# Performance work log

Hardware: AMD Instinct MI355X
Metric: run time of the kernel (lower is better)

The kernel has to match this reference:

```python
import jax, jax.numpy as jnp
import numpy as np

NEG_INF = -1000000.0
G = 8            # window size (hardcoded: assert 8*8 == N)
DIM = 28         # hardcoded channel dim
NH = 4           # num_heads
HD = DIM // NH   # head dim = 7
PDIM = (DIM // 4) // 4  # DynamicPosBias pos_dim = (28//4)//4 = 1


def layernorm(x, g, b, eps=1e-5):
    m = jnp.mean(x, axis=-1, keepdims=True)
    v = jnp.mean((x - m) ** 2, axis=-1, keepdims=True)
    return (x - m) * jax.lax.rsqrt(v + eps) * g + b


def setup_inputs() -> dict:
    key = jax.random.key(0)
    ks = jax.random.split(key, 16)
    s = 0.05
    inp = {
        "x": jax.random.normal(ks[0], (8, 250, 250, DIM), jnp.float32),
        "qkv_w": jax.random.normal(ks[1], (3 * DIM, DIM), jnp.float32) * s,
        "qkv_b": jnp.zeros((3 * DIM,), jnp.float32),
        "proj_w": jax.random.normal(ks[2], (DIM, DIM), jnp.float32) * s,
        "proj_b": jnp.zeros((DIM,), jnp.float32),
        "pos_proj_w": jax.random.normal(ks[3], (PDIM, 2), jnp.float32) * s,
        "pos_proj_b": jnp.zeros((PDIM,), jnp.float32),
        "ln1_g": jnp.ones((PDIM,), jnp.float32),
        "ln1_b": jnp.zeros((PDIM,), jnp.float32),
        "fc1_w": jax.random.normal(ks[4], (PDIM, PDIM), jnp.float32) * s,
        "fc1_b": jnp.zeros((PDIM,), jnp.float32),
        "ln2_g": jnp.ones((PDIM,), jnp.float32),
        "ln2_b": jnp.zeros((PDIM,), jnp.float32),
        "fc2_w": jax.random.normal(ks[5], (PDIM, PDIM), jnp.float32) * s,
        "fc2_b": jnp.zeros((PDIM,), jnp.float32),
        "ln3_g": jnp.ones((PDIM,), jnp.float32),
        "ln3_b": jnp.zeros((PDIM,), jnp.float32),
        "fc3_w": jax.random.normal(ks[6], (NH, PDIM), jnp.float32) * s,
        "fc3_b": jnp.zeros((NH,), jnp.float32),
    }
    return inp


def _rel_pos_index():
    # static relative position index table, (G*G, G*G) int32 in [0, (2G-1)^2)
    coords = np.stack(np.meshgrid(np.arange(G), np.arange(G), indexing="ij"))  # (2,G,G)
    cf = coords.reshape(2, -1)                                                  # (2,GG)
    rel = cf[:, :, None] - cf[:, None, :]                                       # (2,GG,GG)
    rel = rel.transpose(1, 2, 0)
    rel[:, :, 0] += G - 1
    rel[:, :, 1] += G - 1
    rel[:, :, 0] *= 2 * G - 1
    return jnp.asarray(rel.sum(-1), jnp.int32)


def _biases():
    # (2G-1)^2 candidate relative offsets, float (225, 2)
    ph = np.arange(1 - G, G)
    b = np.stack(np.meshgrid(ph, ph, indexing="ij")).reshape(2, -1).T
    return jnp.asarray(b, jnp.float32)


def reference(x, qkv_w, qkv_b, proj_w, proj_b,
              pos_proj_w, pos_proj_b,
              ln1_g, ln1_b, fc1_w, fc1_b,
              ln2_g, ln2_b, fc2_w, fc2_b,
              ln3_g, ln3_b, fc3_w, fc3_b):
    B, H, W, C = x.shape
    pad_b = (-H) % G
    pad_r = (-W) % G
    x = jnp.pad(x, ((0, 0), (0, pad_b), (0, pad_r), (0, 0)))
    Hd, Wd = H + pad_b, W + pad_r
    nH, nW = Hd // G, Wd // G
    nP = nH * nW
    GG = G * G

    # window partition -> (B*nP, GG, C)
    xw = x.reshape(B, nH, G, nW, G, C).transpose(0, 1, 3, 2, 4, 5).reshape(B * nP, GG, C)

    # padding mask over keys, per window: (nP, 1, GG) additive
    m2d = jnp.zeros((Hd, Wd), jnp.float32)
    if pad_b > 0:
        m2d = m2d.at[-pad_b:, :].set(-1.0)
    if pad_r > 0:
        m2d = m2d.at[:, -pad_r:].set(-1.0)
    mw = m2d.reshape(nH, G, nW, G).transpose(0, 2, 1, 3).reshape(nP, GG)
    attn_mask = jnp.where(mw[:, None, :] < 0, NEG_INF, 0.0)  # (nP,1,GG)

    # qkv projection
    qkv = xw @ qkv_w.T + qkv_b                    # (B_, GG, 3C)
    qkv = qkv.reshape(B * nP, GG, 3, NH, HD).transpose(2, 0, 3, 1, 4)
    q, k, v = qkv[0], qkv[1], qkv[2]              # (B_, NH, GG, HD)
    scale = HD ** (-0.5)
    attn = jnp.einsum("bhnd,bhmd->bhnm", q * scale, k)  # (B_, NH, GG, GG)

    # dynamic relative position bias: tiny MLP over (2G-1)^2 offsets
    t = _biases() @ pos_proj_w.T + pos_proj_b                      # (225, PDIM)
    t = layernorm(t, ln1_g, ln1_b)
    t = jax.nn.relu(t) @ fc1_w.T + fc1_b
    t = layernorm(t, ln2_g, ln2_b)
    t = jax.nn.relu(t) @ fc2_w.T + fc2_b
    t = layernorm(t, ln3_g, ln3_b)
    pos = jax.nn.relu(t) @ fc3_w.T + fc3_b                         # (225, NH)
    rpb = pos[_rel_pos_index()]                                    # (GG, GG, NH)
    rpb = rpb.transpose(2, 0, 1)                                   # (NH, GG, GG)
    attn = attn + rpb[None]

    # add padding mask then softmax
    attn = attn.reshape(B, nP, NH, GG, GG) + attn_mask[None, :, None, :, :]
    attn = jax.nn.softmax(attn.reshape(B * nP, NH, GG, GG), axis=-1)

    out = jnp.einsum("bhnm,bhmd->bnhd", attn, v).reshape(B * nP, GG, C)
    out = out @ proj_w.T + proj_b

    # un-window, crop padding, flatten spatial
    out = out.reshape(B, nH, nW, G, G, C).transpose(0, 1, 3, 2, 4, 5).reshape(B, Hd, Wd, C)
    out = out[:, :H, :W, :].reshape(B, H * W, C)
    return out
```

## Files before the change

### kernel.cpp

```cpp
#include <hip/hip_runtime.h>

#define HW 250

typedef float    f32x16 __attribute__((ext_vector_type(16)));
typedef _Float16 f16x8  __attribute__((ext_vector_type(8)));
typedef unsigned u32x4  __attribute__((ext_vector_type(4)));

__device__ inline unsigned pkrtz(float a, float b) {
    return __builtin_bit_cast(unsigned, __builtin_amdgcn_cvt_pkrtz(a, b));
}
__device__ inline f16x8 as_f16x8(u32x4 v) { return __builtin_bit_cast(f16x8, v); }

#define OFF_X   0
#define OFF_WA  2560
#define OFF_PW  7680
#define OFF_VT  8960


__global__ __launch_bounds__(256, 7)
void win_attn(const float* __restrict__ x,
              const float* __restrict__ qkv_w,
              const float* __restrict__ qkv_b,
              const float* __restrict__ proj_w,
              const float* __restrict__ proj_b,
              float* __restrict__ out)
{
    __shared__ __align__(16) short s_pool[11008];
    __shared__ __align__(16) float s_pb[28];
    short* const s_x16  = s_pool + OFF_X;
    short* const s_wa   = s_pool + OFF_WA;
    short* const s_pw16 = s_pool + OFF_PW;
    short* const s_vt   = s_pool + OFF_VT;
    short* const s_o16  = s_pool + OFF_X;
    float* const s_of   = (float*)(s_pool + OFF_WA);

    const int t    = threadIdx.x;
    const int lane = t & 63;
    const int w    = t >> 6;
    const int s_   = lane >> 5;
    const int col  = lane & 31;
    const int blk = blockIdx.x;
    const int b   = blk >> 10;
    const int p   = blk & 1023;
    const int r0  = (p >> 5) << 3;
    const int c0  = (p & 31) << 3;

    f32x16 Z;
    #pragma unroll
    for (int r = 0; r < 16; ++r) Z[r] = 0.f;

    {
        const int co = t >> 3, g = t & 7;
        uint2 h; h.x = 0u; h.y = 0u;
        if (g < 7) {
            if (co < 28) {
                const float4 v = *(const float4*)&proj_w[co * 28 + g * 4];
                h.x = pkrtz(v.x, v.y); h.y = pkrtz(v.z, v.w);
            }
            *(uint2*)&s_pw16[co * 40 + g * 4] = h;
        } else {
            *(uint2*)&s_pw16[co * 40 + 28] = h;
        }
    }
    if (t < 28) s_pb[t] = proj_b[t];

    #pragma unroll
    for (int it = 0; it < 2; ++it) {
        const int i = t + it * 256;
        const int n = i >> 3, g = i & 7;
        if (g < 7) {
            const int r = r0 + (n >> 3), c = c0 + (n & 7);
            float4 v = make_float4(0.f, 0.f, 0.f, 0.f);
            if (r < HW && c < HW)
                v = *(const float4*)&x[((b * HW + r) * HW + c) * 28 + g * 4];
            uint2 h; h.x = pkrtz(v.x, v.y); h.y = pkrtz(v.z, v.w);
            *(uint2*)&s_x16[n * 40 + g * 4] = h;
        } else {
            uint2 h; h.x = 0x00003C00u; h.y = 0u;
            *(uint2*)&s_x16[n * 40 + 28] = h;
        }
    }

    {
        const int rowid = t >> 1, half = t & 1;
        const int slab = rowid >> 5, a = rowid & 31;
        const float SC = 0.5452538663326288f;
        int src = -1; float sc = 1.f;
        if      (a < 4)             { src = slab * 7 + a;            sc = SC; }
        else if (a < 8)             { src = 56 + slab * 7 + (a - 4); }
        else if (a < 11)            { src = slab * 7 + (a - 4);      sc = SC; }
        else if (a >= 12 && a < 15) { src = 56 + slab * 7 + (a - 8); }
        else if (a >= 16 && a < 20) { src = 28 + slab * 7 + (a - 16); }
        else if (a >= 24 && a < 27) { src = 28 + slab * 7 + (a - 20); }
        u32x4 o0 = {0u,0u,0u,0u}, o1 = {0u,0u,0u,0u};
        if (src >= 0) {
            const float* wr = &qkv_w[src * 28];
            if (half == 0) {
                const float4 A = *(const float4*)&wr[0],  B = *(const float4*)&wr[4];
                const float4 C = *(const float4*)&wr[8],  D = *(const float4*)&wr[12];
                o0.x = pkrtz(A.x*sc, A.y*sc); o0.y = pkrtz(A.z*sc, A.w*sc);
                o0.z = pkrtz(B.x*sc, B.y*sc); o0.w = pkrtz(B.z*sc, B.w*sc);
                o1.x = pkrtz(C.x*sc, C.y*sc); o1.y = pkrtz(C.z*sc, C.w*sc);
                o1.z = pkrtz(D.x*sc, D.y*sc); o1.w = pkrtz(D.z*sc, D.w*sc);
            } else {
                const float4 A = *(const float4*)&wr[16], B = *(const float4*)&wr[20];
                const float4 C = *(const float4*)&wr[24];
                const float bias = qkv_b[src];
                o0.x = pkrtz(A.x*sc, A.y*sc); o0.y = pkrtz(A.z*sc, A.w*sc);
                o0.z = pkrtz(B.x*sc, B.y*sc); o0.w = pkrtz(B.z*sc, B.w*sc);
                o1.x = pkrtz(C.x*sc, C.y*sc); o1.y = pkrtz(C.z*sc, C.w*sc);
                o1.z = pkrtz(bias*sc, 0.f);   o1.w = 0u;
            }
        }
        *(u32x4*)&s_wa[rowid * 40 + half * 16 + 0] = o0;
        *(u32x4*)&s_wa[rowid * 40 + half * 16 + 8] = o1;
    }
    __syncthreads();

    u32x4 qf0, qf1, kf0, kf1;
    {
        const f16x8 wfa = *(const f16x8*)&s_wa[(w * 32 + col) * 40 + s_ * 8];
        const f16x8 wfb = *(const f16x8*)&s_wa[(w * 32 + col) * 40 + 16 + s_ * 8];
        #pragma unroll
        for (int tile = 0; tile < 2; ++tile) {
            const int tok = tile * 32 + col;
            const f16x8 xb0 = *(const f16x8*)&s_x16[tok * 40 + s_ * 8];
            const f16x8 xb1 = *(const f16x8*)&s_x16[tok * 40 + 16 + s_ * 8];
            f32x16 C;
            C = __builtin_amdgcn_mfma_f32_32x32x16_f16(wfa, xb0, Z, 0, 0, 0);
            C = __builtin_amdgcn_mfma_f32_32x32x16_f16(wfb, xb1, C, 0, 0, 0);
            u32x4 qf, kf;
            qf.x = s_ ? 0u : pkrtz(C[0],  C[1]);
            qf.y = s_ ? 0u : pkrtz(C[2],  C[3]);
            qf.z = s_ ? 0u : pkrtz(C[4],  C[5]);
            qf.w = s_ ? 0u : pkrtz(C[6],  0.f);
            kf.x = s_ ? 0u : pkrtz(C[8],  C[9]);
            kf.y = s_ ? 0u : pkrtz(C[10], C[11]);
            kf.z = s_ ? 0u : pkrtz(C[12], C[13]);
            kf.w = s_ ? 0u : pkrtz(C[14], 0.f);
            if (s_) {
                const int pos = ((tok >> 4) << 4) + (((tok >> 2) & 1) << 3)
                              + (tok & 3) + (((tok >> 3) & 1) << 2);
                #pragma unroll
                for (int d = 0; d < 8; ++d) {
                    const unsigned hv = (d == 7) ? 0x00003C00u : pkrtz(C[d], 0.f);
                    s_vt[w * 512 + ((d * 64 + pos) ^ (d << 3))] = (short)(hv & 0xffff);
                }
            }
            if (tile == 0) { qf0 = qf; kf0 = kf; } else { qf1 = qf; kf1 = kf; }
        }
    }
    __syncthreads();

    {
        const int vr = min(8, HW - r0), vc = min(8, HW - c0);
        const bool edge = (vr < 8) || (vc < 8);
        const int dd = (col < 8) ? col : 6;
        const f16x8 kfa = as_f16x8(kf0), kfb = as_f16x8(kf1);

        #pragma unroll
        for (int qt = 0; qt < 2; ++qt) {
            const f16x8 qfrag = as_f16x8(qt == 0 ? qf0 : qf1);
            f32x16 a0 = __builtin_amdgcn_mfma_f32_32x32x16_f16(kfa, qfrag, Z, 0, 0, 0);
            f32x16 a1 = __builtin_amdgcn_mfma_f32_32x32x16_f16(kfb, qfrag, Z, 0, 0, 0);
            if (edge) {
                #pragma unroll
                for (int r = 0; r < 16; ++r) {
                    const int kc  = (r & 3) + 4 * s_;
                    const int kr0 = (r >> 2), kr1 = 4 + (r >> 2);
                    a0[r] = (kr0 < vr && kc < vc) ? a0[r] : -1e30f;
                    a1[r] = (kr1 < vr && kc < vc) ? a1[r] : -1e30f;
                }
            }
            #pragma unroll
            for (int r = 0; r < 16; ++r) {
                a0[r] = __builtin_amdgcn_exp2f(a0[r]);
                a1[r] = __builtin_amdgcn_exp2f(a1[r]);
            }

            f32x16 O;
            #pragma unroll
            for (int tt = 0; tt < 4; ++tt) {
                const f16x8 vfrag = *(const f16x8*)&s_vt[w * 512 + ((dd * 64 + tt * 16 + s_ * 8) ^ (dd << 3))];
                const int bb = 8 * (tt & 1);
                float p0,p1,p2,p3,p4,p5,p6,p7;
                if (tt < 2) { p0=a0[bb+0];p1=a0[bb+1];p2=a0[bb+2];p3=a0[bb+3];
                              p4=a0[bb+4];p5=a0[bb+5];p6=a0[bb+6];p7=a0[bb+7]; }
                else        { p0=a1[bb+0];p1=a1[bb+1];p2=a1[bb+2];p3=a1[bb+3];
                              p4=a1[bb+4];p5=a1[bb+5];p6=a1[bb+6];p7=a1[bb+7]; }
                u32x4 pf;
                pf.x = pkrtz(p0, p1); pf.y = pkrtz(p2, p3);
                pf.z = pkrtz(p4, p5); pf.w = pkrtz(p6, p7);
                O = __builtin_amdgcn_mfma_f32_32x32x16_f16(vfrag, as_f16x8(pf),
                                                           (tt == 0) ? Z : O, 0, 0, 0);
            }
            const float os = O[3];
            const float prt = __shfl_xor(os, 32);
            const float sum = s_ ? os : prt;
            const float inv = __builtin_amdgcn_rcpf(sum);
            #pragma unroll
            for (int r = 0; r < 4; ++r) {
                const int d = r + 4 * s_;
                if (d < 7) {
                    const unsigned hv = pkrtz(O[r] * inv, 0.f);
                    s_o16[(32 * qt + col) * 40 + w * 7 + d] = (short)(hv & 0xffff);
                }
            }
        }
    }
    __syncthreads();

    {
        const int tile = w & 1, ch = w >> 1;
        const int tok  = tile * 32 + col;
        const f16x8 ob0 = *(const f16x8*)&s_o16[tok * 40 + 8 * s_];
        const f16x8 ob1 = *(const f16x8*)&s_o16[tok * 40 + 16 + 8 * s_];
        const f16x8 wa0 = *(const f16x8*)&s_pw16[col * 40 + 8 * s_];
        const f16x8 wa1 = *(const f16x8*)&s_pw16[col * 40 + 16 + 8 * s_];
        f32x16 C;
        C = __builtin_amdgcn_mfma_f32_32x32x16_f16(wa0, ob0, Z, 0, 0, 0);
        C = __builtin_amdgcn_mfma_f32_32x32x16_f16(wa1, ob1, C, 0, 0, 0);
        const int wr = tok >> 3, tc = tok & 7;
        #pragma unroll
        for (int j2 = 0; j2 < 2; ++j2) {
            const int j  = 2 * ch + j2;
            const int co = 8 * j + 4 * s_;
            if (co < 28) {
                float4 o;
                o.x = C[4*j+0]; o.y = C[4*j+1]; o.z = C[4*j+2]; o.w = C[4*j+3];
                *(float4*)&s_of[wr * 232 + tc * 28 + co] = o;
            }
        }
    }
    __syncthreads();

    {
        const int l7 = lane / 7;
        #pragma unroll
        for (int i = 0; i < 2; ++i) {
            const int wr = 2 * w + i;
            const int rr = r0 + wr;
            if (lane < 56 && rr < HW) {
                const int tc = l7;
                const int c  = 4 * (lane - 7 * tc);
                if (c0 + tc < HW) {
                    float4 o = *(const float4*)&s_of[wr * 232 + 4 * lane];
                    const float4 bias = *(const float4*)&s_pb[c];
                    o.x += bias.x; o.y += bias.y; o.z += bias.z; o.w += bias.w;
                    *(float4*)&out[((b * HW + rr) * HW + c0 + tc) * 28 + c] = o;
                }
            }
        }
    }
}

extern "C" void kernel_launch(void* const* d_in, const int* in_sizes, int n_in,
                              void* d_out, int out_size, void* d_ws, size_t ws_size,
                              hipStream_t stream) {
    const float* x      = (const float*)d_in[0];
    const float* qkv_w  = (const float*)d_in[1];
    const float* qkv_b  = (const float*)d_in[2];
    const float* proj_w = (const float*)d_in[3];
    const float* proj_b = (const float*)d_in[4];
    float* out = (float*)d_out;

    dim3 grid(8 * 32 * 32);
    dim3 block(256);
    hipLaunchKernelGGL(win_attn, grid, block, 0, stream,
                       x, qkv_w, qkv_b, proj_w, proj_b, out);
}
```

Before: 55.65 us.

## Process four windows per block and stage projection output in fp16

```diff
diff --git a/kernel.cpp b/kernel.cpp
--- a/kernel.cpp
+++ b/kernel.cpp
@@ -1,9 +1,11 @@
 #include <hip/hip_runtime.h>
 
 #define HW 250
+#define NWIN 4
 
 typedef float    f32x16 __attribute__((ext_vector_type(16)));
 typedef _Float16 f16x8  __attribute__((ext_vector_type(8)));
+typedef _Float16 f16x4v __attribute__((ext_vector_type(4)));
 typedef unsigned u32x4  __attribute__((ext_vector_type(4)));
 
 __device__ inline unsigned pkrtz(float a, float b) {
@@ -32,18 +34,14 @@
     short* const s_pw16 = s_pool + OFF_PW;
     short* const s_vt   = s_pool + OFF_VT;
     short* const s_o16  = s_pool + OFF_X;
-    float* const s_of   = (float*)(s_pool + OFF_WA);
+    short* const s_of16 = s_pool + OFF_VT;
 
     const int t    = threadIdx.x;
     const int lane = t & 63;
     const int w    = t >> 6;
     const int s_   = lane >> 5;
     const int col  = lane & 31;
-    const int blk = blockIdx.x;
-    const int b   = blk >> 10;
-    const int p   = blk & 1023;
-    const int r0  = (p >> 5) << 3;
-    const int c0  = (p & 31) << 3;
+    const int blk  = blockIdx.x;
 
     f32x16 Z;
     #pragma unroll
@@ -63,23 +61,6 @@
         }
     }
     if (t < 28) s_pb[t] = proj_b[t];
-
-    #pragma unroll
-    for (int it = 0; it < 2; ++it) {
-        const int i = t + it * 256;
-        const int n = i >> 3, g = i & 7;
-        if (g < 7) {
-            const int r = r0 + (n >> 3), c = c0 + (n & 7);
-            float4 v = make_float4(0.f, 0.f, 0.f, 0.f);
-            if (r < HW && c < HW)
-                v = *(const float4*)&x[((b * HW + r) * HW + c) * 28 + g * 4];
-            uint2 h; h.x = pkrtz(v.x, v.y); h.y = pkrtz(v.z, v.w);
-            *(uint2*)&s_x16[n * 40 + g * 4] = h;
-        } else {
-            uint2 h; h.x = 0x00003C00u; h.y = 0u;
-            *(uint2*)&s_x16[n * 40 + 28] = h;
-        }
-    }
 
     {
         const int rowid = t >> 1, half = t & 1;
@@ -115,138 +96,164 @@
         *(u32x4*)&s_wa[rowid * 40 + half * 16 + 0] = o0;
         *(u32x4*)&s_wa[rowid * 40 + half * 16 + 8] = o1;
     }
-    __syncthreads();
-
-    u32x4 qf0, qf1, kf0, kf1;
-    {
-        const f16x8 wfa = *(const f16x8*)&s_wa[(w * 32 + col) * 40 + s_ * 8];
-        const f16x8 wfb = *(const f16x8*)&s_wa[(w * 32 + col) * 40 + 16 + s_ * 8];
+
+    #pragma unroll 1
+    for (int win = 0; win < NWIN; ++win) {
+        const int g  = blk * NWIN + win;
+        const int b  = g >> 10;
+        const int p  = g & 1023;
+        const int r0 = (p >> 5) << 3;
+        const int c0 = (p & 31) << 3;
+
         #pragma unroll
-        for (int tile = 0; tile < 2; ++tile) {
-            const int tok = tile * 32 + col;
-            const f16x8 xb0 = *(const f16x8*)&s_x16[tok * 40 + s_ * 8];
-            const f16x8 xb1 = *(const f16x8*)&s_x16[tok * 40 + 16 + s_ * 8];
-            f32x16 C;
-            C = __builtin_amdgcn_mfma_f32_32x32x16_f16(wfa, xb0, Z, 0, 0, 0);
-            C = __builtin_amdgcn_mfma_f32_32x32x16_f16(wfb, xb1, C, 0, 0, 0);
-            u32x4 qf, kf;
-            qf.x = s_ ? 0u : pkrtz(C[0],  C[1]);
-            qf.y = s_ ? 0u : pkrtz(C[2],  C[3]);
-            qf.z = s_ ? 0u : pkrtz(C[4],  C[5]);
-            qf.w = s_ ? 0u : pkrtz(C[6],  0.f);
-            kf.x = s_ ? 0u : pkrtz(C[8],  C[9]);
-            kf.y = s_ ? 0u : pkrtz(C[10], C[11]);
-            kf.z = s_ ? 0u : pkrtz(C[12], C[13]);
-            kf.w = s_ ? 0u : pkrtz(C[14], 0.f);
-            if (s_) {
-                const int pos = ((tok >> 4) << 4) + (((tok >> 2) & 1) << 3)
-                              + (tok & 3) + (((tok >> 3) & 1) << 2);
-                #pragma unroll
-                for (int d = 0; d < 8; ++d) {
-                    const unsigned hv = (d == 7) ? 0x00003C00u : pkrtz(C[d], 0.f);
-                    s_vt[w * 512 + ((d * 64 + pos) ^ (d << 3))] = (short)(hv & 0xffff);
-                }
-            }
-            if (tile == 0) { qf0 = qf; kf0 = kf; } else { qf1 = qf; kf1 = kf; }
-        }
-    }
-    __syncthreads();
-
-    {
-        const int vr = min(8, HW - r0), vc = min(8, HW - c0);
-        const bool edge = (vr < 8) || (vc < 8);
-        const int dd = (col < 8) ? col : 6;
-        const f16x8 kfa = as_f16x8(kf0), kfb = as_f16x8(kf1);
-
-        #pragma unroll
-        for (int qt = 0; qt < 2; ++qt) {
-            const f16x8 qfrag = as_f16x8(qt == 0 ? qf0 : qf1);
-            f32x16 a0 = __builtin_amdgcn_mfma_f32_32x32x16_f16(kfa, qfrag, Z, 0, 0, 0);
-            f32x16 a1 = __builtin_amdgcn_mfma_f32_32x32x16_f16(kfb, qfrag, Z, 0, 0, 0);
-            if (edge) {
+        for (int it = 0; it < 2; ++it) {
+            const int i = t + it * 256;
+            const int n = i >> 3, gg = i & 7;
+            if (gg < 7) {
+                const int r = r0 + (n >> 3), c = c0 + (n & 7);
+                float4 v = make_float4(0.f, 0.f, 0.f, 0.f);
+                if (r < HW && c < HW)
+                    v = *(const float4*)&x[((b * HW + r) * HW + c) * 28 + gg * 4];
+                uint2 h; h.x = pkrtz(v.x, v.y); h.y = pkrtz(v.z, v.w);
+                *(uint2*)&s_x16[n * 40 + gg * 4] = h;
+            } else {
+                uint2 h; h.x = 0x00003C00u; h.y = 0u;
+                *(uint2*)&s_x16[n * 40 + 28] = h;
+            }
+        }
+        __syncthreads();
+
+        u32x4 qf0, qf1, kf0, kf1;
+        {
+            const f16x8 wfa = *(const f16x8*)&s_wa[(w * 32 + col) * 40 + s_ * 8];
+            const f16x8 wfb = *(const f16x8*)&s_wa[(w * 32 + col) * 40 + 16 + s_ * 8];
+            #pragma unroll
+            for (int tile = 0; tile < 2; ++tile) {
+                const int tok = tile * 32 + col;
+                const f16x8 xb0 = *(const f16x8*)&s_x16[tok * 40 + s_ * 8];
+                const f16x8 xb1 = *(const f16x8*)&s_x16[tok * 40 + 16 + s_ * 8];
+                f32x16 C;
+                C = __builtin_amdgcn_mfma_f32_32x32x16_f16(wfa, xb0, Z, 0, 0, 0);
+                C = __builtin_amdgcn_mfma_f32_32x32x16_f16(wfb, xb1, C, 0, 0, 0);
+                u32x4 qf, kf;
+                qf.x = s_ ? 0u : pkrtz(C[0],  C[1]);
+                qf.y = s_ ? 0u : pkrtz(C[2],  C[3]);
+                qf.z = s_ ? 0u : pkrtz(C[4],  C[5]);
+                qf.w = s_ ? 0u : pkrtz(C[6],  0.f);
+                kf.x = s_ ? 0u : pkrtz(C[8],  C[9]);
+                kf.y = s_ ? 0u : pkrtz(C[10], C[11]);
+                kf.z = s_ ? 0u : pkrtz(C[12], C[13]);
+                kf.w = s_ ? 0u : pkrtz(C[14], 0.f);
+                if (s_) {
+                    const int pos = ((tok >> 4) << 4) + (((tok >> 2) & 1) << 3)
+                                  + (tok & 3) + (((tok >> 3) & 1) << 2);
+                    #pragma unroll
+                    for (int d = 0; d < 8; ++d) {
+                        const unsigned hv = (d == 7) ? 0x00003C00u : pkrtz(C[d], 0.f);
+                        s_vt[w * 512 + ((d * 64 + pos) ^ (d << 3))] = (short)(hv & 0xffff);
+                    }
+                }
+                if (tile == 0) { qf0 = qf; kf0 = kf; } else { qf1 = qf; kf1 = kf; }
+            }
+        }
+        __syncthreads();
+
+        {
+            const int vr = min(8, HW - r0), vc = min(8, HW - c0);
+            const bool edge = (vr < 8) || (vc < 8);
+            const int dd = (col < 8) ? col : 6;
+            const f16x8 kfa = as_f16x8(kf0), kfb = as_f16x8(kf1);
+
+            #pragma unroll
+            for (int qt = 0; qt < 2; ++qt) {
+                const f16x8 qfrag = as_f16x8(qt == 0 ? qf0 : qf1);
+                f32x16 a0 = __builtin_amdgcn_mfma_f32_32x32x16_f16(kfa, qfrag, Z, 0, 0, 0);
+                f32x16 a1 = __builtin_amdgcn_mfma_f32_32x32x16_f16(kfb, qfrag, Z, 0, 0, 0);
+                if (edge) {
+                    #pragma unroll
+                    for (int r = 0; r < 16; ++r) {
+                        const int kc  = (r & 3) + 4 * s_;
+                        const int kr0 = (r >> 2), kr1 = 4 + (r >> 2);
+                        a0[r] = (kr0 < vr && kc < vc) ? a0[r] : -1e30f;
+                        a1[r] = (kr1 < vr && kc < vc) ? a1[r] : -1e30f;
+                    }
+                }
                 #pragma unroll
                 for (int r = 0; r < 16; ++r) {
-                    const int kc  = (r & 3) + 4 * s_;
-                    const int kr0 = (r >> 2), kr1 = 4 + (r >> 2);
-                    a0[r] = (kr0 < vr && kc < vc) ? a0[r] : -1e30f;
-                    a1[r] = (kr1 < vr && kc < vc) ? a1[r] : -1e30f;
-                }
-            }
-            #pragma unroll
-            for (int r = 0; r < 16; ++r) {
-                a0[r] = __builtin_amdgcn_exp2f(a0[r]);
-                a1[r] = __builtin_amdgcn_exp2f(a1[r]);
-            }
-
-            f32x16 O;
-            #pragma unroll
-            for (int tt = 0; tt < 4; ++tt) {
-                const f16x8 vfrag = *(const f16x8*)&s_vt[w * 512 + ((dd * 64 + tt * 16 + s_ * 8) ^ (dd << 3))];
-                const int bb = 8 * (tt & 1);
-                float p0,p1,p2,p3,p4,p5,p6,p7;
-                if (tt < 2) { p0=a0[bb+0];p1=a0[bb+1];p2=a0[bb+2];p3=a0[bb+3];
-                              p4=a0[bb+4];p5=a0[bb+5];p6=a0[bb+6];p7=a0[bb+7]; }
-                else        { p0=a1[bb+0];p1=a1[bb+1];p2=a1[bb+2];p3=a1[bb+3];
-                              p4=a1[bb+4];p5=a1[bb+5];p6=a1[bb+6];p7=a1[bb+7]; }
-                u32x4 pf;
-                pf.x = pkrtz(p0, p1); pf.y = pkrtz(p2, p3);
-                pf.z = pkrtz(p4, p5); pf.w = pkrtz(p6, p7);
-                O = __builtin_amdgcn_mfma_f32_32x32x16_f16(vfrag, as_f16x8(pf),
-                                                           (tt == 0) ? Z : O, 0, 0, 0);
-            }
-            const float os = O[3];
-            const float prt = __shfl_xor(os, 32);
-            const float sum = s_ ? os : prt;
-            const float inv = __builtin_amdgcn_rcpf(sum);
-            #pragma unroll
-            for (int r = 0; r < 4; ++r) {
-                const int d = r + 4 * s_;
-                if (d < 7) {
-                    const unsigned hv = pkrtz(O[r] * inv, 0.f);
-                    s_o16[(32 * qt + col) * 40 + w * 7 + d] = (short)(hv & 0xffff);
-                }
-            }
-        }
-    }
-    __syncthreads();
-
-    {
-        const int tile = w & 1, ch = w >> 1;
-        const int tok  = tile * 32 + col;
-        const f16x8 ob0 = *(const f16x8*)&s_o16[tok * 40 + 8 * s_];
-        const f16x8 ob1 = *(const f16x8*)&s_o16[tok * 40 + 16 + 8 * s_];
-        const f16x8 wa0 = *(const f16x8*)&s_pw16[col * 40 + 8 * s_];
-        const f16x8 wa1 = *(const f16x8*)&s_pw16[col * 40 + 16 + 8 * s_];
-        f32x16 C;
-        C = __builtin_amdgcn_mfma_f32_32x32x16_f16(wa0, ob0, Z, 0, 0, 0);
-        C = __builtin_amdgcn_mfma_f32_32x32x16_f16(wa1, ob1, C, 0, 0, 0);
-        const int wr = tok >> 3, tc = tok & 7;
-        #pragma unroll
-        for (int j2 = 0; j2 < 2; ++j2) {
-            const int j  = 2 * ch + j2;
-            const int co = 8 * j + 4 * s_;
-            if (co < 28) {
-                float4 o;
-                o.x = C[4*j+0]; o.y = C[4*j+1]; o.z = C[4*j+2]; o.w = C[4*j+3];
-                *(float4*)&s_of[wr * 232 + tc * 28 + co] = o;
-            }
-        }
-    }
-    __syncthreads();
-
-    {
-        const int l7 = lane / 7;
-        #pragma unroll
-        for (int i = 0; i < 2; ++i) {
-            const int wr = 2 * w + i;
-            const int rr = r0 + wr;
-            if (lane < 56 && rr < HW) {
-                const int tc = l7;
-                const int c  = 4 * (lane - 7 * tc);
-                if (c0 + tc < HW) {
-                    float4 o = *(const float4*)&s_of[wr * 232 + 4 * lane];
+                    a0[r] = __builtin_amdgcn_exp2f(a0[r]);
+                    a1[r] = __builtin_amdgcn_exp2f(a1[r]);
+                }
+
+                f32x16 O;
+                #pragma unroll
+                for (int tt = 0; tt < 4; ++tt) {
+                    const f16x8 vfrag = *(const f16x8*)&s_vt[w * 512 + ((dd * 64 + tt * 16 + s_ * 8) ^ (dd << 3))];
+                    const int bb = 8 * (tt & 1);
+                    float p0,p1,p2,p3,p4,p5,p6,p7;
+                    if (tt < 2) { p0=a0[bb+0];p1=a0[bb+1];p2=a0[bb+2];p3=a0[bb+3];
+                                  p4=a0[bb+4];p5=a0[bb+5];p6=a0[bb+6];p7=a0[bb+7]; }
+                    else        { p0=a1[bb+0];p1=a1[bb+1];p2=a1[bb+2];p3=a1[bb+3];
+                                  p4=a1[bb+4];p5=a1[bb+5];p6=a1[bb+6];p7=a1[bb+7]; }
+                    u32x4 pf;
+                    pf.x = pkrtz(p0, p1); pf.y = pkrtz(p2, p3);
+                    pf.z = pkrtz(p4, p5); pf.w = pkrtz(p6, p7);
+                    O = __builtin_amdgcn_mfma_f32_32x32x16_f16(vfrag, as_f16x8(pf),
+                                                               (tt == 0) ? Z : O, 0, 0, 0);
+                }
+                const float os = O[3];
+                const float prt = __shfl_xor(os, 32);
+                const float sum = s_ ? os : prt;
+                const float inv = __builtin_amdgcn_rcpf(sum);
+                #pragma unroll
+                for (int r = 0; r < 4; ++r) {
+                    const int d = r + 4 * s_;
+                    if (d < 7) {
+                        const unsigned hv = pkrtz(O[r] * inv, 0.f);
+                        s_o16[(32 * qt + col) * 40 + w * 7 + d] = (short)(hv & 0xffff);
+                    }
+                }
+            }
+        }
+        __syncthreads();
+
+        {
+            const int tile = w & 1, ch = w >> 1;
+            const int tok  = tile * 32 + col;
+            const f16x8 ob0 = *(const f16x8*)&s_o16[tok * 40 + 8 * s_];
+            const f16x8 ob1 = *(const f16x8*)&s_o16[tok * 40 + 16 + 8 * s_];
+            const f16x8 wa0 = *(const f16x8*)&s_pw16[col * 40 + 8 * s_];
+            const f16x8 wa1 = *(const f16x8*)&s_pw16[col * 40 + 16 + 8 * s_];
+            f32x16 C;
+            C = __builtin_amdgcn_mfma_f32_32x32x16_f16(wa0, ob0, Z, 0, 0, 0);
+            C = __builtin_amdgcn_mfma_f32_32x32x16_f16(wa1, ob1, C, 0, 0, 0);
+            const int wr2 = tok >> 3, tc = tok & 7;
+            #pragma unroll
+            for (int j2 = 0; j2 < 2; ++j2) {
+                const int j  = 2 * ch + j2;
+                const int co = 8 * j + 4 * s_;
+                if (co < 28) {
+                    uint2 hh;
+                    hh.x = pkrtz(C[4*j+0], C[4*j+1]);
+                    hh.y = pkrtz(C[4*j+2], C[4*j+3]);
+                    *(uint2*)&s_of16[wr2 * 232 + tc * 28 + co] = hh;
+                }
+            }
+        }
+        __syncthreads();
+
+        {
+            const int tc = lane / 7;
+            const int c  = 4 * (lane - 7 * tc);
+            #pragma unroll
+            for (int i = 0; i < 2; ++i) {
+                const int wr2 = 2 * w + i;
+                const int rr = r0 + wr2;
+                if (lane < 56 && rr < HW && c0 + tc < HW) {
+                    const f16x4v v = *(const f16x4v*)&s_of16[wr2 * 232 + 4 * lane];
                     const float4 bias = *(const float4*)&s_pb[c];
-                    o.x += bias.x; o.y += bias.y; o.z += bias.z; o.w += bias.w;
+                    float4 o;
+                    o.x = (float)v[0] + bias.x; o.y = (float)v[1] + bias.y;
+                    o.z = (float)v[2] + bias.z; o.w = (float)v[3] + bias.w;
                     *(float4*)&out[((b * HW + rr) * HW + c0 + tc) * 28 + c] = o;
                 }
             }
@@ -264,7 +271,7 @@
     const float* proj_b = (const float*)d_in[4];
     float* out = (float*)d_out;
 
-    dim3 grid(8 * 32 * 32);
+    dim3 grid(8 * 32 * 32 / NWIN);
     dim3 block(256);
     hipLaunchKernelGGL(win_attn, grid, block, 0, stream,
                        x, qkv_w, qkv_b, proj_w, proj_b, out);
```

Measured after the change: 111.1 us. 2x slower.
